# Kernel tuning notes

Hardware: AMD Instinct MI355X
Metric: run time of the kernel (lower is better)

The kernel has to match this reference:

```python
import jax, jax.numpy as jnp
import numpy as np

THRESH = 0.5   # lif_layer_v_threshold
TAU = 0.25     # lif_layer_v_decay
GAMMA = 1.0    # lif_layer_sg_width

@jax.custom_vjp
def spike_fn(v):
    # Heaviside fire with rectangular surrogate gradient (ZIF)
    return (v >= 0).astype(v.dtype)

def _spike_fwd(v):
    return spike_fn(v), v

def _spike_bwd(v, g):
    sg = (jnp.abs(v) < GAMMA / 2).astype(g.dtype) / GAMMA
    return (g * sg,)

spike_fn.defvjp(_spike_fwd, _spike_bwd)

def setup_inputs() -> dict:
    key = jax.random.key(0)
    x = jax.random.normal(key, (32, 16, 128, 32, 32), dtype=jnp.float32)
    return {"x": x}

def reference(x):
    # x: [B, T, C, H, W] -> scan over time with mem kept resident
    xt = jnp.moveaxis(x, 1, 0)            # [T, B, C, H, W]
    mem0 = jnp.zeros_like(xt[0])          # [B, C, H, W]

    def step(mem, x_t):
        mem = mem * TAU + x_t             # leaky integrate
        s = spike_fn(mem - THRESH)        # fire
        mem = (1.0 - s) * mem             # hard reset
        return mem, s

    _, spikes = jax.lax.scan(step, mem0, xt)   # spikes: [T, B, C, H, W]
    return jnp.moveaxis(spikes, 0, 1)          # [B, T, C, H, W]
```

## Files before the change

### kernel.cpp

```cpp
#include <hip/hip_runtime.h>


#define LIF_THRESH 0.5f
#define LIF_TAU    0.25f

typedef float f4 __attribute__((ext_vector_type(4)));

constexpr int T         = 16;
constexpr int CHW       = 128 * 32 * 32;
constexpr int VEC_PER_T = CHW / 4;
constexpr int B         = 32;
constexpr int TOTAL_VEC = B * VEC_PER_T;

__global__ __launch_bounds__(256) void lif_fwd_kernel(
    const f4* __restrict__ x, f4* __restrict__ out)
{
    int tid = blockIdx.x * 256 + threadIdx.x;

    int b     = tid >> 15;
    int inner = tid & (VEC_PER_T - 1);

    size_t base = (size_t)b * (T * VEC_PER_T) + inner;
    const f4* xp = x   + base;
    f4*       op = out + base;

    f4 xt[T];
#pragma unroll
    for (int t = 0; t < T; ++t)
        xt[t] = __builtin_nontemporal_load(&xp[t * VEC_PER_T]);

    float mx = 0.f, my = 0.f, mz = 0.f, mw = 0.f;
#pragma unroll
    for (int t = 0; t < T; ++t) {
        f4 s;

        mx = mx * LIF_TAU + xt[t].x;
        bool fx = (mx >= LIF_THRESH); s.x = fx ? 1.f : 0.f; mx = fx ? 0.f : mx;

        my = my * LIF_TAU + xt[t].y;
        bool fy = (my >= LIF_THRESH); s.y = fy ? 1.f : 0.f; my = fy ? 0.f : my;

        mz = mz * LIF_TAU + xt[t].z;
        bool fz = (mz >= LIF_THRESH); s.z = fz ? 1.f : 0.f; mz = fz ? 0.f : mz;

        mw = mw * LIF_TAU + xt[t].w;
        bool fw = (mw >= LIF_THRESH); s.w = fw ? 1.f : 0.f; mw = fw ? 0.f : mw;

        __builtin_nontemporal_store(s, &op[t * VEC_PER_T]);
    }
}

extern "C" void kernel_launch(void* const* d_in, const int* in_sizes, int n_in,
                              void* d_out, int out_size, void* d_ws, size_t ws_size,
                              hipStream_t stream) {
    const f4* x = (const f4*)d_in[0];
    f4* out = (f4*)d_out;

    const int block = 256;
    const int grid  = TOTAL_VEC / block;

    lif_fwd_kernel<<<grid, block, 0, stream>>>(x, out);
}
```

Baseline: 413.7 us.

## Process four vectors per thread with one-step software-pipelined time loop

Each thread now handles four strided vectors and walks time in a non-unrolled loop, prefetching the next timestep while computing the current one. Launch grid shrinks fourfold. This lowers register use versus loading all sixteen timesteps up front, but reduces outstanding loads per thread and total threads, which may lower memory-level parallelism.

```diff
diff --git a/kernel.cpp b/kernel.cpp
--- a/kernel.cpp
+++ b/kernel.cpp
@@ -6,47 +6,61 @@
 
 typedef float f4 __attribute__((ext_vector_type(4)));
 
-constexpr int T         = 16;
-constexpr int CHW       = 128 * 32 * 32;
-constexpr int VEC_PER_T = CHW / 4;
-constexpr int B         = 32;
-constexpr int TOTAL_VEC = B * VEC_PER_T;
+constexpr int T          = 16;
+constexpr int CHW        = 128 * 32 * 32;
+constexpr int VEC_PER_T  = CHW / 4;
+constexpr int B          = 32;
+constexpr int BLK        = 256;
+constexpr int VPT        = 4;
+constexpr int SEG        = BLK * VPT;
+constexpr int SEGS_PER_B = VEC_PER_T / SEG;
+constexpr int NBLOCKS    = B * SEGS_PER_B;
 
 __global__ __launch_bounds__(256) void lif_fwd_kernel(
     const f4* __restrict__ x, f4* __restrict__ out)
 {
-    int tid = blockIdx.x * 256 + threadIdx.x;
+    const int bid = blockIdx.x;
+    const int b   = bid >> 5;
+    const int seg = bid & (SEGS_PER_B - 1);
 
-    int b     = tid >> 15;
-    int inner = tid & (VEC_PER_T - 1);
-
-    size_t base = (size_t)b * (T * VEC_PER_T) + inner;
+    const size_t base = (size_t)b * (T * VEC_PER_T) + seg * SEG + threadIdx.x;
     const f4* xp = x   + base;
     f4*       op = out + base;
 
-    f4 xt[T];
+    f4 cur[VPT], nxt[VPT], mem[VPT];
+
 #pragma unroll
-    for (int t = 0; t < T; ++t)
-        xt[t] = __builtin_nontemporal_load(&xp[t * VEC_PER_T]);
+    for (int j = 0; j < VPT; ++j) {
+        mem[j] = (f4)(0.f);
+        cur[j] = __builtin_nontemporal_load(&xp[j * BLK]);
+    }
 
-    float mx = 0.f, my = 0.f, mz = 0.f, mw = 0.f;
+#pragma unroll 1
+    for (int t = 0; t < T; ++t) {
+        if (t + 1 < T) {
+            const f4* xq = xp + (t + 1) * VEC_PER_T;
 #pragma unroll
-    for (int t = 0; t < T; ++t) {
-        f4 s;
+            for (int j = 0; j < VPT; ++j)
+                nxt[j] = __builtin_nontemporal_load(&xq[j * BLK]);
+        }
 
-        mx = mx * LIF_TAU + xt[t].x;
-        bool fx = (mx >= LIF_THRESH); s.x = fx ? 1.f : 0.f; mx = fx ? 0.f : mx;
+        f4* oq = op + t * VEC_PER_T;
+#pragma unroll
+        for (int j = 0; j < VPT; ++j) {
+            f4 m = mem[j] * LIF_TAU + cur[j];
+            f4 s;
+            bool fx = (m.x >= LIF_THRESH); s.x = fx ? 1.f : 0.f; m.x = fx ? 0.f : m.x;
+            bool fy = (m.y >= LIF_THRESH); s.y = fy ? 1.f : 0.f; m.y = fy ? 0.f : m.y;
+            bool fz = (m.z >= LIF_THRESH); s.z = fz ? 1.f : 0.f; m.z = fz ? 0.f : m.z;
+            bool fw = (m.w >= LIF_THRESH); s.w = fw ? 1.f : 0.f; m.w = fw ? 0.f : m.w;
+            mem[j] = m;
+            __builtin_nontemporal_store(s, &oq[j * BLK]);
+        }
 
-        my = my * LIF_TAU + xt[t].y;
-        bool fy = (my >= LIF_THRESH); s.y = fy ? 1.f : 0.f; my = fy ? 0.f : my;
-
-        mz = mz * LIF_TAU + xt[t].z;
-        bool fz = (mz >= LIF_THRESH); s.z = fz ? 1.f : 0.f; mz = fz ? 0.f : mz;
-
-        mw = mw * LIF_TAU + xt[t].w;
-        bool fw = (mw >= LIF_THRESH); s.w = fw ? 1.f : 0.f; mw = fw ? 0.f : mw;
-
-        __builtin_nontemporal_store(s, &op[t * VEC_PER_T]);
+        if (t + 1 < T) {
+#pragma unroll
+            for (int j = 0; j < VPT; ++j) cur[j] = nxt[j];
+        }
     }
 }
 
@@ -56,8 +70,5 @@
     const f4* x = (const f4*)d_in[0];
     f4* out = (f4*)d_out;
 
-    const int block = 256;
-    const int grid  = TOTAL_VEC / block;
-
-    lif_fwd_kernel<<<grid, block, 0, stream>>>(x, out);
+    lif_fwd_kernel<<<NBLOCKS, BLK, 0, stream>>>(x, out);
 }
```

After: 437.0 us. 1.06x slower.
